# Performance work log

Hardware: AMD Instinct MI355X
Metric: run time of the kernel (lower is better)

The kernel has to match this reference:

```python
import jax, jax.numpy as jnp
import numpy as np
import math
from jax import lax

EPS = 0.005          # entropic regularization (emdModule eps)
ITERS = 10           # Sinkhorn/auction iterations (emdModule iters)
PERCENTAGES = (0.004, 0.006, 0.008, 0.010, 0.012)
RADIUS = 1.0


def sqdist(a, b):
    # a: (..., N, 3), b: (..., M, 3) -> (..., N, M) squared euclidean distances
    d = (jnp.sum(a * a, -1)[..., :, None]
         + jnp.sum(b * b, -1)[..., None, :]
         - 2.0 * jnp.einsum('...nd,...md->...nm', a, b))
    return jnp.maximum(d, 0.0)


def fps(x, npoint):
    """Furthest point sampling (pn2.furthest_point_sample): starts at index 0."""
    B, N, _ = x.shape
    x = lax.stop_gradient(x)  # indices are non-differentiable

    def body(carry, _):
        dists, far = carry
        centroid = jnp.take_along_axis(x, far[:, None, None], axis=1)  # (B,1,3)
        d = jnp.sum((x - centroid) ** 2, -1)                           # (B,N)
        dists = jnp.minimum(dists, d)
        nxt = jnp.argmax(dists, -1).astype(jnp.int32)
        return (dists, nxt), far

    init = (jnp.full((B, N), 1e10, x.dtype), jnp.zeros((B,), jnp.int32))
    _, idxs = lax.scan(body, init, None, length=npoint)  # (npoint, B)
    return jnp.transpose(idxs)                           # (B, npoint)


def gather_points(pcd, idx):
    # pcd: (B,N,3), idx: (B,K) -> (B,K,3)
    return jnp.take_along_axis(pcd, idx[:, :, None], axis=1)


def emd_approx(x, y, eps, iters):
    """Approximate EMD (emdModule): entropic-regularized assignment between
    equal-size clouds x,y (B,N,3) with uniform marginals; returns per-point
    expected squared distance to the (soft) assignment, shape (B,N)."""
    B, N, _ = x.shape
    C = sqdist(x, y)  # (B,N,N)
    loga = -jnp.log(jnp.asarray(N, C.dtype))

    def body(carry, _):
        f, g = carry
        g = eps * loga - eps * jax.nn.logsumexp((f[:, :, None] - C) / eps, axis=1)
        f = eps * loga - eps * jax.nn.logsumexp((g[:, None, :] - C) / eps, axis=2)
        return (f, g), None

    z = jnp.zeros((B, N), C.dtype)
    (f, g), _ = lax.scan(jax.checkpoint(body), (z, z), None, length=iters)
    logP = (f[:, :, None] + g[:, None, :] - C) / eps  # transport plan (log)
    dist = N * jnp.sum(jnp.exp(logP) * C, axis=2)     # per-point sq distance
    return dist


def chamfer(gt, out):
    d = sqdist(gt, out)        # (B,Ngt,Nout)
    return d.min(2), d.min(1)  # dist per gt point, dist per out point


def uniform_loss(pcd):
    """PU-GAN style get_uniform_loss: FPS seeds + ball query groups, nearest
    intra-group neighbor distance vs expected disk spacing."""
    B, N, _ = pcd.shape
    npoint = int(N * 0.05)
    seeds = gather_points(pcd, fps(pcd, npoint))  # (B,npoint,3)
    d2 = sqdist(seeds, pcd)                       # (B,npoint,N)
    ar = jnp.arange(N)
    loss = jnp.asarray(0.0, pcd.dtype)
    for p in PERCENTAGES:
        nsample = int(N * p)
        r = math.sqrt(p * RADIUS)
        disk_area = math.pi * (RADIUS ** 2) * p / nsample
        expect_len = math.sqrt(disk_area)
        mask = d2 < r * r
        key = jnp.where(mask, ar, N)                     # valid pts keep own idx
        order = jnp.argsort(key, axis=-1)[..., :nsample]  # first nsample in ball
        valid = jnp.take_along_axis(key, order, axis=-1) < N
        idx = jnp.where(valid, order, order[..., :1])     # fill w/ first (pn2 ball_query)
        grouped = pcd[jnp.arange(B)[:, None, None], idx]  # (B,npoint,nsample,3)
        gd = sqdist(grouped, grouped) + jnp.eye(nsample, dtype=pcd.dtype) * 1e10
        nnsq = jnp.min(gd, axis=-1)                       # nearest-neighbor sq dist
        d = jnp.sqrt(jnp.abs(nnsq + 1e-8))
        mean_d = jnp.mean(d, axis=-1)                     # (B,npoint)
        norm = (mean_d - expect_len) ** 2 / (expect_len + 1e-8)
        loss = loss + jnp.mean(norm) * (p * 100.0) ** 2
    return loss / len(PERCENTAGES)


def setup_inputs() -> dict:
    key = jax.random.key(0)
    k1, k2, k3 = jax.random.split(key, 3)
    return {
        'output1': jax.random.uniform(k1, (4, 1024, 3), jnp.float32),
        'output2': jax.random.uniform(k2, (4, 4096, 3), jnp.float32),
        'gt': jax.random.uniform(k3, (4, 4096, 3), jnp.float32),
    }


def reference(output1, output2, gt):
    gt = gt[:, :, :3]
    num_coarse = output1.shape[1]
    # EMD branch
    gt_fps = gather_points(gt, fps(gt, num_coarse))
    emd1 = jnp.sqrt(emd_approx(output1, gt_fps, EPS, ITERS)).mean(1)
    emd2 = jnp.sqrt(emd_approx(output2, gt, EPS, ITERS)).mean(1)
    # Chamfer branch
    d11, d12 = chamfer(gt, output1)
    cd_p1 = (jnp.sqrt(d11).mean(1) + jnp.sqrt(d12).mean(1)) / 2
    cd_t1 = d11.mean(1) + d12.mean(1)
    d21, d22 = chamfer(gt, output2)
    cd_p2 = (jnp.sqrt(d21).mean(1) + jnp.sqrt(d22).mean(1)) / 2
    cd_t2 = d21.mean(1) + d22.mean(1)
    # Uniformity
    u1 = uniform_loss(output1)
    u2 = uniform_loss(output2)
    return (output1, output2, emd1, emd2, cd_p1, cd_p2, cd_t1, cd_t2, u1, u2)
```

## Files before the change

### kernel.cpp

```cpp
#include <hip/hip_runtime.h>
#include <math.h>


extern "C" __device__ float __ocml_native_exp2_f32(float);

__device__ __forceinline__ float sq3_rn(float ax, float ay, float az,
                                        float bx, float by, float bz) {
  float dx = __fsub_rn(ax, bx), dy = __fsub_rn(ay, by), dz = __fsub_rn(az, bz);
  return __fadd_rn(__fadd_rn(__fmul_rn(dx, dx), __fmul_rn(dy, dy)), __fmul_rn(dz, dz));
}

__device__ __forceinline__ float norm3_rn(float x, float y, float z) {
  return __fadd_rn(__fadd_rn(__fmul_rn(x, x), __fmul_rn(y, y)), __fmul_rn(z, z));
}

__device__ __forceinline__ float ex2(float x) {
#if __has_builtin(__builtin_amdgcn_exp2f)
  return __builtin_amdgcn_exp2f(x);
#else
  return __ocml_native_exp2_f32(x);
#endif
}
__device__ __forceinline__ float lg2(float x) { return __builtin_log2f(x); }

#define LOG2E 1.44269504088896340736f
#define LN2   0.69314718055994530942f


__global__ void pack4(const float* __restrict__ out1, const float* __restrict__ out2,
                      const float* __restrict__ gt,
                      float4* __restrict__ X1, float4* __restrict__ X2, float4* __restrict__ Y2,
                      float* __restrict__ outdst, float* __restrict__ sc,
                      float* __restrict__ scr) {
  int i = blockIdx.x * 256 + threadIdx.x;
  if (i < 26) sc[i] = 0.f;
  if (i < 6656) scr[i] = 0.f;
  if (i < 4096) {
    const float* s = out1 + 3 * (size_t)i;
    float x = s[0], y = s[1], z = s[2];
    X1[i] = make_float4(x, y, z, 0.f);
    float* d = outdst + 3 * (size_t)i;
    d[0] = x; d[1] = y; d[2] = z;
  } else if (i < 20480) {
    int j = i - 4096;
    const float* s = out2 + 3 * (size_t)j;
    float x = s[0], y = s[1], z = s[2];
    X2[j] = make_float4(x, y, z, 0.f);
    float* d = outdst + 12288 + 3 * (size_t)j;
    d[0] = x; d[1] = y; d[2] = z;
  } else if (i < 36864) {
    int j = i - 20480;
    const float* s = gt + 3 * (size_t)j;
    Y2[j] = make_float4(s[0], s[1], s[2], 0.f);
  }
}

template <int PPT>
__device__ void fps_body(const float* __restrict__ xb, int it0, int it1,
                         float* __restrict__ dlws, int* __restrict__ farws,
                         bool fresh, bool save,
                         float4* __restrict__ y1g, int* __restrict__ idxg,
                         float* spx, float* spy, float* spz,
                         int* obs, unsigned long long* red ) {
  int t = threadIdx.x;
  float rx[PPT], ry[PPT], rz[PPT], dl[PPT];
#pragma unroll
  for (int j = 0; j < PPT; ++j) {
    int n = t + (j << 9);
    float x = xb[3 * n], y = xb[3 * n + 1], z = xb[3 * n + 2];
    rx[j] = x; ry[j] = y; rz[j] = z;
    spx[n] = x; spy[n] = y; spz[n] = z;
  }
  if (fresh) {
#pragma unroll
    for (int j = 0; j < PPT; ++j) dl[j] = 1e10f;
  } else {
#pragma unroll
    for (int j = 0; j < PPT; ++j) dl[j] = dlws[(j << 9) + t];
  }
  int far = fresh ? 0 : farws[0];
  if (fresh && t == 0) {
    if (y1g) y1g[0] = make_float4(xb[0], xb[1], xb[2], 0.f);
    if (idxg) idxg[0] = 0;
  }
  __syncthreads();
  int lane = t & 63, wid = t >> 6;
  for (int it = it0; it < it1; ++it) {
    float cx = spx[far], cy = spy[far], cz = spz[far];
    float bv = -1.f; int bi = 0;
#pragma unroll
    for (int j = 0; j < PPT; ++j) {
      int n = t + (j << 9);
      float d = sq3_rn(rx[j], ry[j], rz[j], cx, cy, cz);
      float dn = fminf(dl[j], d);
      dl[j] = dn;
      bool c = dn > bv;
      bv = c ? dn : bv;
      bi = c ? n : bi;
    }
    unsigned long long key =
        ((unsigned long long)__float_as_uint(bv) << 32) | (unsigned)(0x7fffffff - bi);
#pragma unroll
    for (int off = 1; off <= 32; off <<= 1) {
      unsigned long long k2 = __shfl_xor(key, off);
      key = (k2 > key) ? k2 : key;
    }
    unsigned long long* rb = red + ((it & 1) << 3);
    if (lane == 0) rb[wid] = key;
    __syncthreads();
    unsigned long long k0 = rb[0], k1 = rb[1], k2 = rb[2], k3 = rb[3];
    unsigned long long k4 = rb[4], k5 = rb[5], k6 = rb[6], k7 = rb[7];
    unsigned long long a0 = k0 > k1 ? k0 : k1, a1 = k2 > k3 ? k2 : k3;
    unsigned long long a2 = k4 > k5 ? k4 : k5, a3 = k6 > k7 ? k6 : k7;
    unsigned long long b0 = a0 > a1 ? a0 : a1, b1 = a2 > a3 ? a2 : a3;
    unsigned long long kk = b0 > b1 ? b0 : b1;
    far = 0x7fffffff - (int)(unsigned)(kk & 0xffffffffULL);
    if (t == 0) obs[it - it0] = far;
  }
  __syncthreads();
  int cnt = it1 - it0;
  if (y1g)
    for (int i = t; i < cnt; i += 512) {
      int j = obs[i];
      y1g[it0 + i] = make_float4(spx[j], spy[j], spz[j], 0.f);
    }
  if (idxg)
    for (int i = t; i < cnt; i += 512) idxg[it0 + i] = obs[i];
  if (save) {
#pragma unroll
    for (int j = 0; j < PPT; ++j) dlws[(j << 9) + t] = dl[j];
    if (t == 0) farws[0] = far;
  }
}

__device__ void chamfer_wave2(const float4* __restrict__ A, const float4* __restrict__ Bp,
                              int Na, int Nb, int w, int lane,
                              float* __restrict__ scr, int sp_s, int st_s, int slot) {
  int rows = Na >> 1;
  int b = w / rows, i0 = (w - b * rows) << 1;
  float4 a0 = A[(size_t)b * Na + i0];
  float4 a1 = A[(size_t)b * Na + i0 + 1];
  const float4* pb = Bp + (size_t)b * Nb;
  float mn0 = 3.4e38f, mn1 = 3.4e38f;
  for (int j = lane; j < Nb; j += 64) {
    float4 p = pb[j];
    float dx0 = p.x - a0.x, dy0 = p.y - a0.y, dz0 = p.z - a0.z;
    mn0 = fminf(mn0, dx0 * dx0 + dy0 * dy0 + dz0 * dz0);
    float dx1 = p.x - a1.x, dy1 = p.y - a1.y, dz1 = p.z - a1.z;
    mn1 = fminf(mn1, dx1 * dx1 + dy1 * dy1 + dz1 * dz1);
  }
  for (int off = 32; off; off >>= 1) {
    mn0 = fminf(mn0, __shfl_xor(mn0, off));
    mn1 = fminf(mn1, __shfl_xor(mn1, off));
  }
  if (lane == 0) {
    atomicAdd(&scr[(sp_s + b) * 256 + slot], 0.5f * (sqrtf(mn0) + sqrtf(mn1)) * (1.f / (float)Na));
    atomicAdd(&scr[(st_s + b) * 256 + slot], (mn0 + mn1) * (1.f / (float)Na));
  }
}

struct Mega1Args {
  const float *gt, *out1, *out2;
  const float4 *X1, *X2, *Y2;
  float4* Y1;
  float* dlws; int* farws;
  int* idx_u1; int* idx_u2;
  float* scr;
  int gt_it1;
};

__global__ __launch_bounds__(512) void mega1(Mega1Args A) {
  __shared__ __align__(16) unsigned char sm[55296];
  float* spx = (float*)sm;
  float* spy = (float*)(sm + 16384);
  float* spz = (float*)(sm + 32768);
  int* obs = (int*)(sm + 49152);
  unsigned long long* red = (unsigned long long*)(sm + 53248);
  int blk = blockIdx.x;
  int t = threadIdx.x;
  if (blk < 4) {
    __builtin_amdgcn_s_setprio(3);
    int b = blk;
    fps_body<8>(A.gt + (size_t)b * 4096 * 3, 1, A.gt_it1,
                A.dlws + (size_t)b * 4096, A.farws + b, true, true,
                A.Y1 + (size_t)b * 1024, nullptr, spx, spy, spz, obs, red);
    return;
  }
  if (blk < 8) {
    __builtin_amdgcn_s_setprio(3);
    int b = blk - 4;
    fps_body<8>(A.out2 + (size_t)b * 4096 * 3, 1, 204, nullptr, nullptr, true, false,
                nullptr, A.idx_u2 + (size_t)b * 204, spx, spy, spz, obs, red);
    return;
  }
  if (blk < 12) {
    __builtin_amdgcn_s_setprio(3);
    int b = blk - 8;
    fps_body<2>(A.out1 + (size_t)b * 1024 * 3, 1, 51, nullptr, nullptr, true, false,
                nullptr, A.idx_u1 + (size_t)b * 51, spx, spy, spz, obs, red);
    return;
  }
  __builtin_amdgcn_s_setprio(0);
  int lane = t & 63, wid = t >> 6;
  int slot = ((blk << 3) + wid) & 255;
  int wt = (blk - 12) * 8 + wid;
  if (wt < 8192)        chamfer_wave2(A.Y2, A.X1, 4096, 1024, wt,         lane, A.scr, 8, 16, slot);
  else if (wt < 10240)  chamfer_wave2(A.X1, A.Y2, 1024, 4096, wt - 8192,  lane, A.scr, 8, 16, slot);
  else if (wt < 18432)  chamfer_wave2(A.Y2, A.X2, 4096, 4096, wt - 10240, lane, A.scr, 12, 20, slot);
  else                  chamfer_wave2(A.X2, A.Y2, 4096, 4096, wt - 18432, lane, A.scr, 12, 20, slot);
}

__device__ void sink_wave8(float4* __restrict__ Pout, const float4* __restrict__ Pred,
                           int N, float c, int w0, float ie2, float eps_ln2,
                           float* xs, float* ys, float* zs, float* ws4, int nthr) {
  int t = threadIdx.x, lane = t & 63;
  int b = w0 / N, o0 = w0 - b * N;
  float qx[8], qy[8], qz[8], Bc[8], S[8];
  float two_ie = 2.f * ie2;
#pragma unroll
  for (int r = 0; r < 8; ++r) {
    float4 m = Pout[(size_t)b * N + o0 + r];
    qx[r] = two_ie * m.x; qy[r] = two_ie * m.y; qz[r] = two_ie * m.z;
    Bc[r] = -ie2 * (m.x * m.x + m.y * m.y + m.z * m.z);
    S[r] = 0.f;
  }
  const float4* Rb = Pred + (size_t)b * N;
  for (int base = 0; base < N; base += 1024) {
    __syncthreads();
    for (int i = t; i < 1024; i += nthr) {
      float4 p = Rb[base + i];
      xs[i] = p.x; ys[i] = p.y; zs[i] = p.z;
      ws4[i] = (p.w - fmaf(p.z, p.z, fmaf(p.y, p.y, p.x * p.x))) * ie2;
    }
    __syncthreads();
#pragma unroll
    for (int k = 0; k < 16; ++k) {
      int idx = lane + (k << 6);
      float px = xs[idx], py = ys[idx], pz = zs[idx], pw = ws4[idx];
#pragma unroll
      for (int r = 0; r < 8; ++r)
        S[r] += ex2(fmaf(pz, qz[r], fmaf(py, qy[r], fmaf(px, qx[r], pw + Bc[r]))));
    }
  }
#pragma unroll
  for (int r = 0; r < 8; ++r)
    for (int off = 32; off; off >>= 1) S[r] += __shfl_xor(S[r], off);
  if (lane == 0) {
#pragma unroll
    for (int r = 0; r < 8; ++r)
      Pout[(size_t)b * N + o0 + r].w = c - eps_ln2 * lg2(S[r]);
  }
}

__device__ void emd_dist_wave(const float4* __restrict__ X, const float4* __restrict__ Y,
                              int N, int task, int lane, float ie2,
                              float* __restrict__ scr, int base_s, int slot) {
  int b = task / N, n = task - b * N;
  float4 mine = X[(size_t)b * N + n];
  const float4* Yb = Y + (size_t)b * N;
  float acc = 0.f;
  for (int m = lane; m < N; m += 64) {
    float4 p = Yb[m];
    float dx = p.x - mine.x, dy = p.y - mine.y, dz = p.z - mine.z;
    float d = dx * dx + dy * dy + dz * dz;
    acc += ex2((mine.w + p.w - d) * ie2) * d;
  }
  for (int off = 32; off; off >>= 1) acc += __shfl_xor(acc, off);
  if (lane == 0)
    atomicAdd(&scr[(base_s + b) * 256 + slot], sqrtf((float)N * acc) * (1.f / (float)N));
}

struct UniP {
  float r2[5]; int ns[5]; float exden[5]; float exlen[5]; float wg[5];
};

__device__ void uniform_wave(const float* __restrict__ pcd, const int* __restrict__ fpsidx,
                             int N, int npoint, const UniP& P, int task, int lane,
                             int* sel, float* gx, float* gy, float* gz,
                             float* __restrict__ scr, int us, int slot) {
  int pi = task % 5;
  int tmp = task / 5;
  int s = tmp % npoint;
  int b = tmp / npoint;
  int nsample = P.ns[pi];
  float r2 = P.r2[pi];
  const float* Pb = pcd + (size_t)b * N * 3;
  int sidx = fpsidx[b * npoint + s];
  float sx = Pb[3 * sidx], sy = Pb[3 * sidx + 1], sz = Pb[3 * sidx + 2];
  float snorm = norm3_rn(sx, sy, sz);

  int cnt = 0;
  for (int base = 0; base < N && cnt < nsample; base += 64) {
    int n = base + lane;
    float pxn = Pb[3 * n], pyn = Pb[3 * n + 1], pzn = Pb[3 * n + 2];
    float pn2 = norm3_rn(pxn, pyn, pzn);
    float dot = __fadd_rn(__fadd_rn(__fmul_rn(sx, pxn), __fmul_rn(sy, pyn)), __fmul_rn(sz, pzn));
    float d2 = fmaxf(__fsub_rn(__fadd_rn(snorm, pn2), __fmul_rn(2.f, dot)), 0.f);
    unsigned long long bal = __ballot(d2 < r2);
    while (bal && cnt < nsample) {
      int bit = __builtin_ctzll(bal);
      if (lane == 0) sel[cnt] = base + bit;
      cnt++;
      bal &= bal - 1;
    }
  }
  if (lane < nsample) {
    int gi = (lane < cnt) ? sel[lane] : sel[0];
    gx[lane] = Pb[3 * gi]; gy[lane] = Pb[3 * gi + 1]; gz[lane] = Pb[3 * gi + 2];
  }
  float dval = 0.f;
  if (lane < nsample) {
    float mn = 1e10f;
    for (int k = 0; k < nsample; ++k) {
      if (k == lane) continue;
      float dx = gx[lane] - gx[k], dy = gy[lane] - gy[k], dz = gz[lane] - gz[k];
      float d = dx * dx + dy * dy + dz * dz;
      mn = fminf(mn, d);
    }
    dval = sqrtf(fabsf(mn + 1e-8f));
  }
  for (int off = 32; off; off >>= 1) dval += __shfl_xor(dval, off);
  if (lane == 0) {
    float mean_d = dval / (float)nsample;
    float diff = mean_d - P.exlen[pi];
    atomicAdd(&scr[us * 256 + slot], diff * diff / P.exden[pi] * P.wg[pi]);
  }
}

struct SinkUArgs {
  float4* Pout; const float4* Pred; int N; float c; int nfps, nsink;
  const float* gt; float* dlws; int* farws; float4* Y1;
  int it0, it1;
  const float4 *dX, *dY; int dN, dbase, d2_0, d2_n;
  const float *o1raw, *o2raw;
  const int *iu1, *iu2;
  UniP P1, P2;
  int uni0;
  float* scr;
  float ie2, eps_ln2;
};

__global__ __launch_bounds__(512) void sinku(SinkUArgs A) {
  __shared__ __align__(16) unsigned char sm[55296];
  int blk = blockIdx.x;
  int t = threadIdx.x, lane = t & 63, wid = t >> 6;
  if (blk < A.nfps) {
    __builtin_amdgcn_s_setprio(3);
    float* spx = (float*)sm;
    float* spy = (float*)(sm + 16384);
    float* spz = (float*)(sm + 32768);
    int* obs = (int*)(sm + 49152);
    unsigned long long* red = (unsigned long long*)(sm + 53248);
    int b = blk;
    fps_body<8>(A.gt + (size_t)b * 4096 * 3, A.it0, A.it1,
                A.dlws + (size_t)b * 4096, A.farws + b, false, true,
                A.Y1 + (size_t)b * 1024, nullptr, spx, spy, spz, obs, red);
    return;
  }
  __builtin_amdgcn_s_setprio(0);
  float* smf = (float*)sm;
  if (blk < A.nfps + A.nsink) {
    int sblk = blk - A.nfps;
    int w0 = ((sblk << 3) + wid) << 3;
    sink_wave8(A.Pout, A.Pred, A.N, A.c, w0, A.ie2, A.eps_ln2,
               smf, smf + 1024, smf + 2048, smf + 3072, 512);
    return;
  }
  int slot = ((blk << 3) + wid) & 255;
  if (blk < A.nfps + A.nsink + A.d2_n) {
    int dblk = A.d2_0 + (blk - A.nfps - A.nsink);
    emd_dist_wave(A.dX, A.dY, A.dN, dblk * 8 + wid, lane, A.ie2, A.scr, A.dbase, slot);
    return;
  }
  int ublk = blk - (A.nfps + A.nsink + A.d2_n);
  int task = (A.uni0 + ublk) * 8 + wid;
  float* sl = smf + wid * 256;
  int* sel = (int*)sl;
  float* gx = smf + 2048 + wid * 256;
  float* gy = smf + 4096 + wid * 256;
  float* gz = smf + 6144 + wid * 256;
  if (task < 1020)
    uniform_wave(A.o1raw, A.iu1, 1024, 51, A.P1, task, lane, sel, gx, gy, gz, A.scr, 24, slot);
  else if (task < 5100)
    uniform_wave(A.o2raw, A.iu2, 4096, 204, A.P2, task - 1020, lane, sel, gx, gy, gz, A.scr, 25, slot);
}

__global__ __launch_bounds__(256) void dist1(const float4* __restrict__ X1,
                                             const float4* __restrict__ Y1,
                                             float* __restrict__ scr, float ie2) {
  int lane = threadIdx.x & 63, wid = threadIdx.x >> 6;
  int slot = ((blockIdx.x << 2) + wid) & 255;
  emd_dist_wave(X1, Y1, 1024, blockIdx.x * 4 + wid, lane, ie2, scr, 0, slot);
}

__global__ __launch_bounds__(256) void reduce_sc(const float* __restrict__ scr,
                                                 float* __restrict__ sc) {
  __shared__ float r4[4];
  int t = threadIdx.x, lane = t & 63, wid = t >> 6;
  for (int s = 0; s < 26; ++s) {
    float v = scr[s * 256 + t];
    for (int off = 32; off; off >>= 1) v += __shfl_xor(v, off);
    if (lane == 0) r4[wid] = v;
    __syncthreads();
    if (t == 0) sc[s] = r4[0] + r4[1] + r4[2] + r4[3];
    __syncthreads();
  }
}


extern "C" void kernel_launch(void* const* d_in, const int* in_sizes, int n_in,
                              void* d_out, int out_size, void* d_ws, size_t ws_size,
                              hipStream_t stream) {
  const float* out1 = (const float*)d_in[0];
  const float* out2 = (const float*)d_in[1];
  const float* gt   = (const float*)d_in[2];
  float* out = (float*)d_out;
  const int B = 4, N1 = 1024, N2 = 4096;

  char* ws = (char*)d_ws;
  float*  dl_ws  = (float*)(ws + 0);
  int*    far_ws = (int*)(ws + 64 * 1024);
  int*    idx_u1 = (int*)(ws + 66 * 1024);
  int*    idx_u2 = (int*)(ws + 68 * 1024);
  float*  scr    = (float*)(ws + 80 * 1024);
  float4* X1 = (float4*)(ws + 112 * 1024);
  float4* Y1 = (float4*)(ws + 176 * 1024);
  float4* X2 = (float4*)(ws + 240 * 1024);
  float4* Y2 = (float4*)(ws + 496 * 1024);

  float* sc = out + (size_t)B * N1 * 3 + (size_t)B * N2 * 3;

  pack4<<<(36864 + 255) / 256, 256, 0, stream>>>(out1, out2, gt, X1, X2, Y2, out, sc, scr);

  const float ie2 = 200.0f * LOG2E;
  const float eps_ln2 = 0.005f * LN2;
  float c1 = (float)(0.005 * (-log((double)N1)));
  float c2 = (float)(0.005 * (-log((double)N2)));

  const int GT_M = 204, CH2 = 41;

  Mega1Args M1;
  M1.gt = gt; M1.out1 = out1; M1.out2 = out2;
  M1.X1 = X1; M1.X2 = X2; M1.Y2 = Y2; M1.Y1 = Y1;
  M1.dlws = dl_ws; M1.farws = far_ws;
  M1.idx_u1 = idx_u1; M1.idx_u2 = idx_u2; M1.scr = scr;
  M1.gt_it1 = GT_M;
  mega1<<<12 + 3328, 512, 0, stream>>>(M1);

  const double PCT[5] = {0.004, 0.006, 0.008, 0.01, 0.012};
  int np1 = 51, np2 = 204;
  UniP P1, P2;
  for (int k = 0; k < 5; ++k) {
    double p = PCT[k];
    {
      int ns = (int)((double)N1 * p);
      double r = sqrt(p * 1.0);
      double el = sqrt(M_PI * 1.0 * p / (double)ns);
      P1.r2[k] = (float)(r * r); P1.ns[k] = ns;
      P1.exlen[k] = (float)el;   P1.exden[k] = (float)(el + 1e-8);
      P1.wg[k] = (float)((p * 100.0) * (p * 100.0) / (5.0 * (double)B * (double)np1));
    }
    {
      int ns = (int)((double)N2 * p);
      double r = sqrt(p * 1.0);
      double el = sqrt(M_PI * 1.0 * p / (double)ns);
      P2.r2[k] = (float)(r * r); P2.ns[k] = ns;
      P2.exlen[k] = (float)el;   P2.exden[k] = (float)(el + 1e-8);
      P2.wg[k] = (float)((p * 100.0) * (p * 100.0) / (5.0 * (double)B * (double)np2));
    }
  }

  SinkUArgs SA;
  SA.gt = gt; SA.dlws = dl_ws; SA.farws = far_ws; SA.Y1 = Y1;
  SA.ie2 = ie2; SA.eps_ln2 = eps_ln2;
  SA.o1raw = out1; SA.o2raw = out2; SA.iu1 = idx_u1; SA.iu2 = idx_u2;
  SA.P1 = P1; SA.P2 = P2; SA.scr = scr;
  SA.dX = X2; SA.dY = Y2; SA.dN = N2; SA.dbase = 4;

  const int UNI_BLOCKS = 638;
  SA.N = N2; SA.c = c2; SA.nfps = 4; SA.nsink = 256; SA.d2_0 = 0; SA.d2_n = 0;
  int chunk = 0, uni_done = 0;
  for (int it = 0; it < 10; ++it) {
    for (int half = 0; half < 2; ++half) {
      SA.Pout = half ? X2 : Y2;
      SA.Pred = half ? (const float4*)Y2 : (const float4*)X2;
      SA.it0 = GT_M + CH2 * chunk;
      SA.it1 = SA.it0 + CH2;
      chunk++;
      int un = 0;
      if (uni_done < UNI_BLOCKS) un = (UNI_BLOCKS - uni_done < 213) ? UNI_BLOCKS - uni_done : 213;
      SA.uni0 = uni_done;
      uni_done += un;
      sinku<<<4 + 256 + un, 512, 0, stream>>>(SA);
    }
  }

  SA.N = N1; SA.c = c1; SA.nfps = 0; SA.nsink = 64;
  SA.it0 = 0; SA.it1 = 0;
  int d2_done = 0;
  for (int it = 0; it < 10; ++it) {
    for (int half = 0; half < 2; ++half) {
      SA.Pout = half ? X1 : Y1;
      SA.Pred = half ? (const float4*)Y1 : (const float4*)X1;
      int dn = (2048 - d2_done < 103) ? 2048 - d2_done : 103;
      SA.d2_0 = d2_done; SA.d2_n = dn;
      d2_done += dn;
      SA.uni0 = UNI_BLOCKS;
      sinku<<<64 + dn, 512, 0, stream>>>(SA);
    }
  }

  dist1<<<1024, 256, 0, stream>>>(X1, Y1, scr, ie2);
  reduce_sc<<<1, 256, 0, stream>>>(scr, sc);
}
```

Before: 1.202 ms.

## Carry winner coordinates through FPS reduction instead of staging the cloud in LDS

Furthest point sampling no longer copies the whole point cloud into shared memory to look up the next centroid. Each lane carries the coordinates of its best candidate through the argmax, and the winning wave publishes them alongside the key so every thread reads the next centroid from a small LDS slot. The winning lane also writes the sampled point and index directly each iteration, which removes the trailing gather loop. In mega1, LDS shrinks from about 54 KB to 512 bytes, which may raise occupancy for the co-resident chamfer blocks. The cost is extra selects and stores in the serial FPS loop.

```diff
diff --git a/kernel.cpp b/kernel.cpp
--- a/kernel.cpp
+++ b/kernel.cpp
@@ -60,16 +60,13 @@
                          float* __restrict__ dlws, int* __restrict__ farws,
                          bool fresh, bool save,
                          float4* __restrict__ y1g, int* __restrict__ idxg,
-                         float* spx, float* spy, float* spz,
-                         int* obs, unsigned long long* red ) {
+                         unsigned long long* red, float4* redc, float4* bcf) {
   int t = threadIdx.x;
   float rx[PPT], ry[PPT], rz[PPT], dl[PPT];
 #pragma unroll
   for (int j = 0; j < PPT; ++j) {
     int n = t + (j << 9);
-    float x = xb[3 * n], y = xb[3 * n + 1], z = xb[3 * n + 2];
-    rx[j] = x; ry[j] = y; rz[j] = z;
-    spx[n] = x; spy[n] = y; spz[n] = z;
+    rx[j] = xb[3 * n]; ry[j] = xb[3 * n + 1]; rz[j] = xb[3 * n + 2];
   }
   if (fresh) {
 #pragma unroll
@@ -83,11 +80,13 @@
     if (y1g) y1g[0] = make_float4(xb[0], xb[1], xb[2], 0.f);
     if (idxg) idxg[0] = 0;
   }
+  if (t == 0) *bcf = make_float4(xb[3 * far], xb[3 * far + 1], xb[3 * far + 2], 0.f);
   __syncthreads();
-  int lane = t & 63, wid = t >> 6;
+  float4 cc = *bcf;
   for (int it = it0; it < it1; ++it) {
-    float cx = spx[far], cy = spy[far], cz = spz[far];
+    float cx = cc.x, cy = cc.y, cz = cc.z;
     float bv = -1.f; int bi = 0;
+    float bx = 0.f, by = 0.f, bz = 0.f;
 #pragma unroll
     for (int j = 0; j < PPT; ++j) {
       int n = t + (j << 9);
@@ -97,35 +96,46 @@
       bool c = dn > bv;
       bv = c ? dn : bv;
       bi = c ? n : bi;
+      bx = c ? rx[j] : bx;
+      by = c ? ry[j] : by;
+      bz = c ? rz[j] : bz;
     }
     unsigned long long key =
         ((unsigned long long)__float_as_uint(bv) << 32) | (unsigned)(0x7fffffff - bi);
+    unsigned long long kmine = key;
 #pragma unroll
     for (int off = 1; off <= 32; off <<= 1) {
       unsigned long long k2 = __shfl_xor(key, off);
       key = (k2 > key) ? k2 : key;
     }
-    unsigned long long* rb = red + ((it & 1) << 3);
-    if (lane == 0) rb[wid] = key;
+    int bb = (it & 1) << 3;
+    int wid = t >> 6;
+    if (kmine == key) {
+      red[bb + wid] = key;
+      redc[bb + wid] = make_float4(bx, by, bz, 0.f);
+    }
     __syncthreads();
-    unsigned long long k0 = rb[0], k1 = rb[1], k2 = rb[2], k3 = rb[3];
-    unsigned long long k4 = rb[4], k5 = rb[5], k6 = rb[6], k7 = rb[7];
+    unsigned long long k0 = red[bb + 0], k1 = red[bb + 1], k2 = red[bb + 2], k3 = red[bb + 3];
+    unsigned long long k4 = red[bb + 4], k5 = red[bb + 5], k6 = red[bb + 6], k7 = red[bb + 7];
     unsigned long long a0 = k0 > k1 ? k0 : k1, a1 = k2 > k3 ? k2 : k3;
     unsigned long long a2 = k4 > k5 ? k4 : k5, a3 = k6 > k7 ? k6 : k7;
     unsigned long long b0 = a0 > a1 ? a0 : a1, b1 = a2 > a3 ? a2 : a3;
     unsigned long long kk = b0 > b1 ? b0 : b1;
     far = 0x7fffffff - (int)(unsigned)(kk & 0xffffffffULL);
-    if (t == 0) obs[it - it0] = far;
-  }
-  __syncthreads();
-  int cnt = it1 - it0;
-  if (y1g)
-    for (int i = t; i < cnt; i += 512) {
-      int j = obs[i];
-      y1g[it0 + i] = make_float4(spx[j], spy[j], spz[j], 0.f);
-    }
-  if (idxg)
-    for (int i = t; i < cnt; i += 512) idxg[it0 + i] = obs[i];
+    int wstar = 0;
+    wstar = (k1 == kk) ? 1 : wstar;
+    wstar = (k2 == kk) ? 2 : wstar;
+    wstar = (k3 == kk) ? 3 : wstar;
+    wstar = (k4 == kk) ? 4 : wstar;
+    wstar = (k5 == kk) ? 5 : wstar;
+    wstar = (k6 == kk) ? 6 : wstar;
+    wstar = (k7 == kk) ? 7 : wstar;
+    cc = redc[bb + wstar];
+    if (kmine == kk) {
+      if (y1g) y1g[it] = make_float4(bx, by, bz, 0.f);
+      if (idxg) idxg[it] = far;
+    }
+  }
   if (save) {
 #pragma unroll
     for (int j = 0; j < PPT; ++j) dlws[(j << 9) + t] = dl[j];
@@ -170,12 +180,10 @@
 };
 
 __global__ __launch_bounds__(512) void mega1(Mega1Args A) {
-  __shared__ __align__(16) unsigned char sm[55296];
-  float* spx = (float*)sm;
-  float* spy = (float*)(sm + 16384);
-  float* spz = (float*)(sm + 32768);
-  int* obs = (int*)(sm + 49152);
-  unsigned long long* red = (unsigned long long*)(sm + 53248);
+  __shared__ __align__(16) unsigned char sm[512];
+  unsigned long long* red = (unsigned long long*)sm;
+  float4* redc = (float4*)(sm + 128);
+  float4* bcf = (float4*)(sm + 384);
   int blk = blockIdx.x;
   int t = threadIdx.x;
   if (blk < 4) {
@@ -183,21 +191,21 @@
     int b = blk;
     fps_body<8>(A.gt + (size_t)b * 4096 * 3, 1, A.gt_it1,
                 A.dlws + (size_t)b * 4096, A.farws + b, true, true,
-                A.Y1 + (size_t)b * 1024, nullptr, spx, spy, spz, obs, red);
+                A.Y1 + (size_t)b * 1024, nullptr, red, redc, bcf);
     return;
   }
   if (blk < 8) {
     __builtin_amdgcn_s_setprio(3);
     int b = blk - 4;
     fps_body<8>(A.out2 + (size_t)b * 4096 * 3, 1, 204, nullptr, nullptr, true, false,
-                nullptr, A.idx_u2 + (size_t)b * 204, spx, spy, spz, obs, red);
+                nullptr, A.idx_u2 + (size_t)b * 204, red, redc, bcf);
     return;
   }
   if (blk < 12) {
     __builtin_amdgcn_s_setprio(3);
     int b = blk - 8;
     fps_body<2>(A.out1 + (size_t)b * 1024 * 3, 1, 51, nullptr, nullptr, true, false,
-                nullptr, A.idx_u1 + (size_t)b * 51, spx, spy, spz, obs, red);
+                nullptr, A.idx_u1 + (size_t)b * 51, red, redc, bcf);
     return;
   }
   __builtin_amdgcn_s_setprio(0);
@@ -346,15 +354,13 @@
   int t = threadIdx.x, lane = t & 63, wid = t >> 6;
   if (blk < A.nfps) {
     __builtin_amdgcn_s_setprio(3);
-    float* spx = (float*)sm;
-    float* spy = (float*)(sm + 16384);
-    float* spz = (float*)(sm + 32768);
-    int* obs = (int*)(sm + 49152);
-    unsigned long long* red = (unsigned long long*)(sm + 53248);
+    unsigned long long* red = (unsigned long long*)sm;
+    float4* redc = (float4*)(sm + 128);
+    float4* bcf = (float4*)(sm + 384);
     int b = blk;
     fps_body<8>(A.gt + (size_t)b * 4096 * 3, A.it0, A.it1,
                 A.dlws + (size_t)b * 4096, A.farws + b, false, true,
-                A.Y1 + (size_t)b * 1024, nullptr, spx, spy, spz, obs, red);
+                A.Y1 + (size_t)b * 1024, nullptr, red, redc, bcf);
     return;
   }
   __builtin_amdgcn_s_setprio(0);
```

Result: slower. 1.387 ms (+15.4%).

## Co-schedule N1 Sinkhorn half-steps with N2 sinkhorn launches and rebalance FPS chunks

Applied to the files above, without the earlier changes.

Restructures the launch schedule so that the first ten half-iterations of the small (N=1024) Sinkhorn problem run in the same launches as the last ten half-iterations of the large problem, via a second sink block range in sinku. FPS is now spread over the first ten launches with doubled chunks, and the EMD distance work for the large problem is spread over ten launches instead of twenty. The goal is to cut the total launch count and fill idle CUs while the large problem runs. In exchange the co-scheduled launches are heavier, and FPS chunks per launch are larger, which may lengthen the critical path.

```diff
diff --git a/kernel.cpp b/kernel.cpp
--- a/kernel.cpp
+++ b/kernel.cpp
@@ -329,6 +329,7 @@
 
 struct SinkUArgs {
   float4* Pout; const float4* Pred; int N; float c; int nfps, nsink;
+  float4* Pout_b; const float4* Pred_b; int Nb; float cb; int nsink_b;
   const float* gt; float* dlws; int* farws; float4* Y1;
   int it0, it1;
   const float4 *dX, *dY; int dN, dbase, d2_0, d2_n;
@@ -359,20 +360,28 @@
   }
   __builtin_amdgcn_s_setprio(0);
   float* smf = (float*)sm;
-  if (blk < A.nfps + A.nsink) {
-    int sblk = blk - A.nfps;
-    int w0 = ((sblk << 3) + wid) << 3;
+  int rb = blk - A.nfps;
+  if (rb < A.nsink) {
+    int w0 = ((rb << 3) + wid) << 3;
     sink_wave8(A.Pout, A.Pred, A.N, A.c, w0, A.ie2, A.eps_ln2,
                smf, smf + 1024, smf + 2048, smf + 3072, 512);
     return;
   }
+  rb -= A.nsink;
+  if (rb < A.nsink_b) {
+    int w0 = ((rb << 3) + wid) << 3;
+    sink_wave8(A.Pout_b, A.Pred_b, A.Nb, A.cb, w0, A.ie2, A.eps_ln2,
+               smf, smf + 1024, smf + 2048, smf + 3072, 512);
+    return;
+  }
+  rb -= A.nsink_b;
   int slot = ((blk << 3) + wid) & 255;
-  if (blk < A.nfps + A.nsink + A.d2_n) {
-    int dblk = A.d2_0 + (blk - A.nfps - A.nsink);
+  if (rb < A.d2_n) {
+    int dblk = A.d2_0 + rb;
     emd_dist_wave(A.dX, A.dY, A.dN, dblk * 8 + wid, lane, A.ie2, A.scr, A.dbase, slot);
     return;
   }
-  int ublk = blk - (A.nfps + A.nsink + A.d2_n);
+  int ublk = rb - A.d2_n;
   int task = (A.uni0 + ublk) * 8 + wid;
   float* sl = smf + wid * 256;
   int* sel = (int*)sl;
@@ -437,7 +446,7 @@
   float c1 = (float)(0.005 * (-log((double)N1)));
   float c2 = (float)(0.005 * (-log((double)N2)));
 
-  const int GT_M = 204, CH2 = 41;
+  const int GT_M = 204, CH2 = 82;
 
   Mega1Args M1;
   M1.gt = gt; M1.out1 = out1; M1.out2 = out2;
@@ -478,36 +487,42 @@
   SA.dX = X2; SA.dY = Y2; SA.dN = N2; SA.dbase = 4;
 
   const int UNI_BLOCKS = 638;
-  SA.N = N2; SA.c = c2; SA.nfps = 4; SA.nsink = 256; SA.d2_0 = 0; SA.d2_n = 0;
-  int chunk = 0, uni_done = 0;
-  for (int it = 0; it < 10; ++it) {
-    for (int half = 0; half < 2; ++half) {
-      SA.Pout = half ? X2 : Y2;
-      SA.Pred = half ? (const float4*)Y2 : (const float4*)X2;
-      SA.it0 = GT_M + CH2 * chunk;
-      SA.it1 = SA.it0 + CH2;
-      chunk++;
-      int un = 0;
-      if (uni_done < UNI_BLOCKS) un = (UNI_BLOCKS - uni_done < 213) ? UNI_BLOCKS - uni_done : 213;
-      SA.uni0 = uni_done;
-      uni_done += un;
-      sinku<<<4 + 256 + un, 512, 0, stream>>>(SA);
-    }
-  }
-
-  SA.N = N1; SA.c = c1; SA.nfps = 0; SA.nsink = 64;
-  SA.it0 = 0; SA.it1 = 0;
+  SA.N = N2; SA.c = c2; SA.nfps = 4; SA.nsink = 256;
+  SA.nsink_b = 0; SA.Pout_b = nullptr; SA.Pred_b = nullptr; SA.Nb = N1; SA.cb = c1;
+  SA.d2_0 = 0; SA.d2_n = 0;
+  int uni_done = 0;
+  for (int h = 0; h < 10; ++h) {
+    SA.Pout = (h & 1) ? X2 : Y2;
+    SA.Pred = (h & 1) ? (const float4*)Y2 : (const float4*)X2;
+    SA.it0 = GT_M + CH2 * h;
+    SA.it1 = SA.it0 + CH2;
+    int un = 0;
+    if (uni_done < UNI_BLOCKS) un = (UNI_BLOCKS - uni_done < 213) ? UNI_BLOCKS - uni_done : 213;
+    SA.uni0 = uni_done;
+    uni_done += un;
+    sinku<<<4 + 256 + un, 512, 0, stream>>>(SA);
+  }
+
+  SA.nfps = 0; SA.it0 = 0; SA.it1 = 0; SA.uni0 = UNI_BLOCKS;
+  SA.nsink_b = 64;
+  for (int h = 10; h < 20; ++h) {
+    SA.Pout = (h & 1) ? X2 : Y2;
+    SA.Pred = (h & 1) ? (const float4*)Y2 : (const float4*)X2;
+    int h1 = h - 10;
+    SA.Pout_b = (h1 & 1) ? X1 : Y1;
+    SA.Pred_b = (h1 & 1) ? (const float4*)Y1 : (const float4*)X1;
+    sinku<<<256 + 64, 512, 0, stream>>>(SA);
+  }
+
+  SA.nsink = 64; SA.N = N1; SA.c = c1; SA.nsink_b = 0;
   int d2_done = 0;
-  for (int it = 0; it < 10; ++it) {
-    for (int half = 0; half < 2; ++half) {
-      SA.Pout = half ? X1 : Y1;
-      SA.Pred = half ? (const float4*)Y1 : (const float4*)X1;
-      int dn = (2048 - d2_done < 103) ? 2048 - d2_done : 103;
-      SA.d2_0 = d2_done; SA.d2_n = dn;
-      d2_done += dn;
-      SA.uni0 = UNI_BLOCKS;
-      sinku<<<64 + dn, 512, 0, stream>>>(SA);
-    }
+  for (int h1 = 10; h1 < 20; ++h1) {
+    SA.Pout = (h1 & 1) ? X1 : Y1;
+    SA.Pred = (h1 & 1) ? (const float4*)Y1 : (const float4*)X1;
+    int dn = (2048 - d2_done < 205) ? 2048 - d2_done : 205;
+    SA.d2_0 = d2_done; SA.d2_n = dn;
+    d2_done += dn;
+    sinku<<<64 + dn, 512, 0, stream>>>(SA);
   }
 
   dist1<<<1024, 256, 0, stream>>>(X1, Y1, scr, ie2);
```

Result: slower. 1.305 ms (+8.6%).

## Replace EMD1 tail kernel launches with one cooperative persistent kernel using grid sync

Applied to the files above, without the earlier changes.

The 20 small EMD1 Sinkhorn half-iteration launches, the dist1 launch and the reduce launch become a single cooperative kernel. Inside it, grid.sync replaces the kernel boundaries, and the EMD2 distance work is spread across the blocks left idle by the 64 Sinkhorn blocks. This targets launch overhead and tail gaps between the many small launches. In exchange it adds grid-wide barrier costs, and it depends on all 256 blocks of 512 threads being co-resident.

```diff
diff --git a/kernel.cpp b/kernel.cpp
--- a/kernel.cpp
+++ b/kernel.cpp
@@ -1,5 +1,8 @@
 #include <hip/hip_runtime.h>
+#include <hip/hip_cooperative_groups.h>
 #include <math.h>
+
+namespace cg = cooperative_groups;
 
 
 extern "C" __device__ float __ocml_native_exp2_f32(float);
@@ -331,7 +334,6 @@
   float4* Pout; const float4* Pred; int N; float c; int nfps, nsink;
   const float* gt; float* dlws; int* farws; float4* Y1;
   int it0, it1;
-  const float4 *dX, *dY; int dN, dbase, d2_0, d2_n;
   const float *o1raw, *o2raw;
   const int *iu1, *iu2;
   UniP P1, P2;
@@ -367,12 +369,7 @@
     return;
   }
   int slot = ((blk << 3) + wid) & 255;
-  if (blk < A.nfps + A.nsink + A.d2_n) {
-    int dblk = A.d2_0 + (blk - A.nfps - A.nsink);
-    emd_dist_wave(A.dX, A.dY, A.dN, dblk * 8 + wid, lane, A.ie2, A.scr, A.dbase, slot);
-    return;
-  }
-  int ublk = blk - (A.nfps + A.nsink + A.d2_n);
+  int ublk = blk - (A.nfps + A.nsink);
   int task = (A.uni0 + ublk) * 8 + wid;
   float* sl = smf + wid * 256;
   int* sel = (int*)sl;
@@ -385,25 +382,51 @@
     uniform_wave(A.o2raw, A.iu2, 4096, 204, A.P2, task - 1020, lane, sel, gx, gy, gz, A.scr, 25, slot);
 }
 
-__global__ __launch_bounds__(256) void dist1(const float4* __restrict__ X1,
-                                             const float4* __restrict__ Y1,
-                                             float* __restrict__ scr, float ie2) {
-  int lane = threadIdx.x & 63, wid = threadIdx.x >> 6;
-  int slot = ((blockIdx.x << 2) + wid) & 255;
-  emd_dist_wave(X1, Y1, 1024, blockIdx.x * 4 + wid, lane, ie2, scr, 0, slot);
-}
-
-__global__ __launch_bounds__(256) void reduce_sc(const float* __restrict__ scr,
-                                                 float* __restrict__ sc) {
-  __shared__ float r4[4];
-  int t = threadIdx.x, lane = t & 63, wid = t >> 6;
-  for (int s = 0; s < 26; ++s) {
-    float v = scr[s * 256 + t];
-    for (int off = 32; off; off >>= 1) v += __shfl_xor(v, off);
-    if (lane == 0) r4[wid] = v;
-    __syncthreads();
-    if (t == 0) sc[s] = r4[0] + r4[1] + r4[2] + r4[3];
-    __syncthreads();
+struct TailArgs {
+  float4 *X1, *Y1;
+  const float4 *X2, *Y2;
+  float c1, ie2, eps_ln2;
+  float* scr;
+  float* sc;
+};
+
+__global__ __launch_bounds__(512) void emd1_tail(TailArgs A) {
+  cg::grid_group grid = cg::this_grid();
+  __shared__ __align__(16) float smf[4096];
+  int blk = blockIdx.x, t = threadIdx.x, lane = t & 63, wid = t >> 6;
+  int slot = ((blk << 3) + wid) & 255;
+  for (int h = 0; h < 20; ++h) {
+    if (blk < 64) {
+      float4* Pout = (h & 1) ? A.X1 : A.Y1;
+      const float4* Pred = (h & 1) ? (const float4*)A.Y1 : (const float4*)A.X1;
+      int w0 = ((blk << 3) + wid) << 3;
+      sink_wave8(Pout, Pred, 1024, A.c1, w0, A.ie2, A.eps_ln2,
+                 smf, smf + 1024, smf + 2048, smf + 3072, 512);
+    } else {
+      int task = h * 1536 + (blk - 64) * 8 + wid;
+      if (task < 16384)
+        emd_dist_wave(A.X2, A.Y2, 4096, task, lane, A.ie2, A.scr, 4, slot);
+    }
+    __threadfence();
+    grid.sync();
+  }
+  {
+    int w = (blk << 3) + wid;
+    emd_dist_wave(A.X1, A.Y1, 1024, w, lane, A.ie2, A.scr, 0, w & 255);
+    emd_dist_wave(A.X1, A.Y1, 1024, w + 2048, lane, A.ie2, A.scr, 0, (w + 2048) & 255);
+  }
+  __threadfence();
+  grid.sync();
+  if (blk == 0) {
+    float* r4 = smf;
+    for (int s = 0; s < 26; ++s) {
+      float v = (t < 256) ? A.scr[s * 256 + t] : 0.f;
+      for (int off = 32; off; off >>= 1) v += __shfl_xor(v, off);
+      if (lane == 0 && t < 256) r4[wid] = v;
+      __syncthreads();
+      if (t == 0) A.sc[s] = r4[0] + r4[1] + r4[2] + r4[3];
+      __syncthreads();
+    }
   }
 }
 
@@ -475,10 +498,9 @@
   SA.ie2 = ie2; SA.eps_ln2 = eps_ln2;
   SA.o1raw = out1; SA.o2raw = out2; SA.iu1 = idx_u1; SA.iu2 = idx_u2;
   SA.P1 = P1; SA.P2 = P2; SA.scr = scr;
-  SA.dX = X2; SA.dY = Y2; SA.dN = N2; SA.dbase = 4;
 
   const int UNI_BLOCKS = 638;
-  SA.N = N2; SA.c = c2; SA.nfps = 4; SA.nsink = 256; SA.d2_0 = 0; SA.d2_n = 0;
+  SA.N = N2; SA.c = c2; SA.nfps = 4; SA.nsink = 256;
   int chunk = 0, uni_done = 0;
   for (int it = 0; it < 10; ++it) {
     for (int half = 0; half < 2; ++half) {
@@ -495,21 +517,10 @@
     }
   }
 
-  SA.N = N1; SA.c = c1; SA.nfps = 0; SA.nsink = 64;
-  SA.it0 = 0; SA.it1 = 0;
-  int d2_done = 0;
-  for (int it = 0; it < 10; ++it) {
-    for (int half = 0; half < 2; ++half) {
-      SA.Pout = half ? X1 : Y1;
-      SA.Pred = half ? (const float4*)Y1 : (const float4*)X1;
-      int dn = (2048 - d2_done < 103) ? 2048 - d2_done : 103;
-      SA.d2_0 = d2_done; SA.d2_n = dn;
-      d2_done += dn;
-      SA.uni0 = UNI_BLOCKS;
-      sinku<<<64 + dn, 512, 0, stream>>>(SA);
-    }
-  }
-
-  dist1<<<1024, 256, 0, stream>>>(X1, Y1, scr, ie2);
-  reduce_sc<<<1, 256, 0, stream>>>(scr, sc);
-}
+  TailArgs TA;
+  TA.X1 = X1; TA.Y1 = Y1; TA.X2 = X2; TA.Y2 = Y2;
+  TA.c1 = c1; TA.ie2 = ie2; TA.eps_ln2 = eps_ln2;
+  TA.scr = scr; TA.sc = sc;
+  void* targs[] = {(void*)&TA};
+  hipLaunchCooperativeKernel((void*)emd1_tail, dim3(256), dim3(512), targs, 0, stream);
+}
```

Measured after the change: 2.699 ms. 2.25x slower.
